# Optimization experiments

Measured on AMD Instinct MI355X. Metric: run time of the kernel, lower is better.

Reference implementation:

```python
import jax, jax.numpy as jnp
import numpy as np

V = 200000  # num entities
R = 100     # num relations
D = 128     # embedding_dim
K = 20      # entity_neighbor_num
B = 128     # batch (docs)
N = 50      # entities per doc


def setup_inputs() -> dict:
    key = jax.random.key(0)
    ks = jax.random.split(key, 8)
    return {
        "entity_ids": jax.random.randint(ks[0], (B, N), 0, V),
        "adj_entity": jax.random.randint(ks[1], (V, K), 0, V),
        "adj_relation": jax.random.randint(ks[2], (V, K), 0, R),
        "entity_embedding": jax.random.normal(ks[3], (V, D), jnp.float32),
        "relation_embedding": jax.random.normal(ks[4], (R, D), jnp.float32),
        "W_att": jax.random.normal(ks[5], (3 * D, 1), jnp.float32) * 0.05,
        "b_att": jnp.zeros((1,), jnp.float32),
        "W_conv": jax.random.normal(ks[6], (2 * D, D), jnp.float32) * 0.05,
        "b_conv": jnp.zeros((D,), jnp.float32),
    }


def reference(entity_ids, adj_entity, adj_relation, entity_embedding,
              relation_embedding, W_att, b_att, W_conv, b_conv):
    # neighbor ids: [B, N, K]
    neigh_ent = adj_entity[entity_ids]
    neigh_rel = adj_relation[entity_ids]
    ne = entity_embedding[neigh_ent]      # [B, N, K, D]
    nr = relation_embedding[neigh_rel]    # [B, N, K, D]
    ee = entity_embedding[entity_ids]     # [B, N, D]
    ee_exp = jnp.broadcast_to(ee[:, :, None, :], ne.shape)  # [B, N, K, D]
    concat = jnp.concatenate([ee_exp, ne, nr], axis=-1)     # [B, N, K, 3D]
    logits = jax.nn.relu(concat @ W_att + b_att)            # [B, N, K, 1]
    # NOTE: faithful to original nn.Softmax(dim=0) -> softmax over batch axis
    att = jax.nn.softmax(logits, axis=0)                    # [B, N, K, 1]
    neighbor_att = jnp.sum(att * ne, axis=2)                # [B, N, D]
    agg_in = jnp.concatenate([ee, neighbor_att], axis=-1)   # [B, N, 2D]
    return jax.nn.relu(agg_in @ W_conv + b_conv)            # [B, N, D]
```

## Files before the change

### kernel.cpp

```cpp
#include <hip/hip_runtime.h>

#define V 200000
#define R 100
#define D 128
#define K 20
#define B 128
#define N 50

__global__ void k_logits(const int* __restrict__ eids,
                         const int* __restrict__ adjE,
                         const int* __restrict__ adjR,
                         const float* __restrict__ EE,
                         const float* __restrict__ RE,
                         const float* __restrict__ Watt,
                         const float* __restrict__ batt,
                         float* __restrict__ att) {
  const int lane = threadIdx.x & 63;
  const int wv   = threadIdx.x >> 6;
  const int bn   = blockIdx.x * 4 + wv;
  const int b = bn / N;
  const int n = bn % N;
  const int eid = eids[bn];

  const float2 wa_e = ((const float2*)Watt)[lane];
  const float2 e2   = ((const float2*)(EE + (size_t)eid * D))[lane];
  float p = e2.x * wa_e.x + e2.y * wa_e.y;
  #pragma unroll
  for (int off = 32; off > 0; off >>= 1) p += __shfl_down(p, off);
  const float s_ee = __shfl(p, 0) + batt[0];

  const int g  = lane >> 4;
  const int sl = lane & 15;
  const float4* wnp = (const float4*)(Watt + D + 8 * sl);
  const float4* wrp = (const float4*)(Watt + 2 * D + 8 * sl);
  const float4 wn0 = wnp[0], wn1 = wnp[1];
  const float4 wr0 = wrp[0], wr1 = wrp[1];

  const int* ae = adjE + eid * K;
  const int* ar = adjR + eid * K;

  float q[5];
  #pragma unroll
  for (int k5 = 0; k5 < 5; ++k5) {
    const int k = k5 * 4 + g;
    const int nid = ae[k];
    const int rid = ar[k];
    const float4* np = (const float4*)(EE + (size_t)nid * D + 8 * sl);
    const float4* rp = (const float4*)(RE + (size_t)rid * D + 8 * sl);
    const float4 n0 = np[0], n1 = np[1];
    const float4 r0 = rp[0], r1 = rp[1];
    float s = n0.x * wn0.x + n0.y * wn0.y + n0.z * wn0.z + n0.w * wn0.w
            + n1.x * wn1.x + n1.y * wn1.y + n1.z * wn1.z + n1.w * wn1.w
            + r0.x * wr0.x + r0.y * wr0.y + r0.z * wr0.z + r0.w * wr0.w
            + r1.x * wr1.x + r1.y * wr1.y + r1.z * wr1.z + r1.w * wr1.w;
    #pragma unroll
    for (int off = 8; off > 0; off >>= 1) s += __shfl_down(s, off, 16);
    q[k5] = s;
  }

  if (sl == 0) {
    #pragma unroll
    for (int k5 = 0; k5 < 5; ++k5) {
      const int k = k5 * 4 + g;
      const float logit = s_ee + q[k5];
      att[(n * K + k) * B + b] = logit > 0.0f ? logit : 0.0f;
    }
  }
}

__global__ void k_softmax(float* __restrict__ att) {
  __shared__ float red[4];
  const int gg = blockIdx.x;
  const int t = threadIdx.x;
  const float x = att[gg * B + t];

  float m = x;
  #pragma unroll
  for (int off = 32; off > 0; off >>= 1) m = fmaxf(m, __shfl_down(m, off));
  if ((t & 63) == 0) red[t >> 6] = m;
  __syncthreads();
  const float mm = fmaxf(red[0], red[1]);

  const float e = __expf(x - mm);
  float s = e;
  #pragma unroll
  for (int off = 32; off > 0; off >>= 1) s += __shfl_down(s, off);
  if ((t & 63) == 0) red[2 + (t >> 6)] = s;
  __syncthreads();
  const float ss = red[2] + red[3];

  att[gg * B + t] = e / ss;
}

#define G 8
__global__ void k_out(const int* __restrict__ eids,
                      const int* __restrict__ adjE,
                      const float* __restrict__ EE,
                      const float* __restrict__ att,
                      const float* __restrict__ Wc,
                      const float* __restrict__ bc,
                      float* __restrict__ out) {
  __shared__ float agg[G][2 * D];
  __shared__ float part[2][G][D];
  __shared__ float s_att[G][K];
  __shared__ int   s_nid[G][K];

  const int t = threadIdx.x;
  const int d = t & 127;
  const int h = t >> 7;
  const int base = blockIdx.x * G;

  if (t < G * K) {
    const int j = t / K, k = t % K;
    const int bn = base + j;
    const int b = bn / N;
    const int n = bn % N;
    const int eid = eids[bn];
    s_nid[j][k] = adjE[eid * K + k];
    s_att[j][k] = att[(n * K + k) * B + b];
  }
  __syncthreads();

  #pragma unroll
  for (int jj = 0; jj < G / 2; ++jj) {
    const int j = h + jj * 2;
    const int bn = base + j;
    const int eid = eids[bn];
    const float ee = EE[(size_t)eid * D + d];
    float na = 0.0f;
    #pragma unroll
    for (int k = 0; k < K; ++k)
      na += s_att[j][k] * EE[(size_t)s_nid[j][k] * D + d];
    agg[j][d] = ee;
    agg[j][D + d] = na;
  }
  __syncthreads();

  float acc[G];
  #pragma unroll
  for (int j = 0; j < G; ++j) acc[j] = 0.0f;
  const int ibase = h * D;
  for (int c = 0; c < 32; ++c) {
    const int i = ibase + c * 4;
    const float w0 = Wc[(i + 0) * D + d];
    const float w1 = Wc[(i + 1) * D + d];
    const float w2 = Wc[(i + 2) * D + d];
    const float w3 = Wc[(i + 3) * D + d];
    #pragma unroll
    for (int j = 0; j < G; ++j) {
      const float4 a = *(const float4*)&agg[j][i];
      acc[j] += a.x * w0 + a.y * w1 + a.z * w2 + a.w * w3;
    }
  }
  #pragma unroll
  for (int j = 0; j < G; ++j) part[h][j][d] = acc[j];
  __syncthreads();

  const float bb = bc[d];
  #pragma unroll
  for (int jj = 0; jj < G / 2; ++jj) {
    const int j = h + jj * 2;
    const float v = part[0][j][d] + part[1][j][d] + bb;
    out[(size_t)(base + j) * D + d] = v > 0.0f ? v : 0.0f;
  }
}

extern "C" void kernel_launch(void* const* d_in, const int* in_sizes, int n_in,
                              void* d_out, int out_size, void* d_ws, size_t ws_size,
                              hipStream_t stream) {
  const int*   eids = (const int*)d_in[0];
  const int*   adjE = (const int*)d_in[1];
  const int*   adjR = (const int*)d_in[2];
  const float* EE   = (const float*)d_in[3];
  const float* RE   = (const float*)d_in[4];
  const float* Watt = (const float*)d_in[5];
  const float* batt = (const float*)d_in[6];
  const float* Wc   = (const float*)d_in[7];
  const float* bc   = (const float*)d_in[8];
  float* out = (float*)d_out;

  float* att = (float*)d_ws;

  k_logits<<<(B * N) / 4, 256, 0, stream>>>(eids, adjE, adjR, EE, RE, Watt,
                                            batt, att);
  k_softmax<<<N * K, 128, 0, stream>>>(att);
  k_out<<<(B * N) / G, 256, 0, stream>>>(eids, adjE, EE, att, Wc, bc, out);
}
```

Before: 206.3 us.

## Precompute per-entity attention scores and fuse the logit gather into softmax

The attention logit is linear in the concatenated input, so it splits into per-entity and per-relation dot products with slices of W_att. A new kernel computes these scalar scores for every entity and relation by streaming the whole tables sequentially. The softmax kernel then builds each logit from three scalar lookups instead of gathering full 128-wide neighbor and relation rows. This swaps a random gather of about 128k rows for a sequential read of all 200k entity rows, plus extra workspace for the score arrays.

```diff
diff --git a/kernel.cpp b/kernel.cpp
--- a/kernel.cpp
+++ b/kernel.cpp
@@ -7,89 +7,72 @@
 #define B 128
 #define N 50
 
-__global__ void k_logits(const int* __restrict__ eids,
-                         const int* __restrict__ adjE,
-                         const int* __restrict__ adjR,
-                         const float* __restrict__ EE,
+__global__ void k_scores(const float* __restrict__ EE,
                          const float* __restrict__ RE,
                          const float* __restrict__ Watt,
-                         const float* __restrict__ batt,
-                         float* __restrict__ att) {
+                         float* __restrict__ s0,
+                         float* __restrict__ s1,
+                         float* __restrict__ s2) {
   const int lane = threadIdx.x & 63;
-  const int wv   = threadIdx.x >> 6;
-  const int bn   = blockIdx.x * 4 + wv;
-  const int b = bn / N;
-  const int n = bn % N;
-  const int eid = eids[bn];
-
-  const float2 wa_e = ((const float2*)Watt)[lane];
-  const float2 e2   = ((const float2*)(EE + (size_t)eid * D))[lane];
-  float p = e2.x * wa_e.x + e2.y * wa_e.y;
-  #pragma unroll
-  for (int off = 32; off > 0; off >>= 1) p += __shfl_down(p, off);
-  const float s_ee = __shfl(p, 0) + batt[0];
-
-  const int g  = lane >> 4;
-  const int sl = lane & 15;
-  const float4* wnp = (const float4*)(Watt + D + 8 * sl);
-  const float4* wrp = (const float4*)(Watt + 2 * D + 8 * sl);
-  const float4 wn0 = wnp[0], wn1 = wnp[1];
-  const float4 wr0 = wrp[0], wr1 = wrp[1];
-
-  const int* ae = adjE + eid * K;
-  const int* ar = adjR + eid * K;
-
-  float q[5];
-  #pragma unroll
-  for (int k5 = 0; k5 < 5; ++k5) {
-    const int k = k5 * 4 + g;
-    const int nid = ae[k];
-    const int rid = ar[k];
-    const float4* np = (const float4*)(EE + (size_t)nid * D + 8 * sl);
-    const float4* rp = (const float4*)(RE + (size_t)rid * D + 8 * sl);
-    const float4 n0 = np[0], n1 = np[1];
-    const float4 r0 = rp[0], r1 = rp[1];
-    float s = n0.x * wn0.x + n0.y * wn0.y + n0.z * wn0.z + n0.w * wn0.w
-            + n1.x * wn1.x + n1.y * wn1.y + n1.z * wn1.z + n1.w * wn1.w
-            + r0.x * wr0.x + r0.y * wr0.y + r0.z * wr0.z + r0.w * wr0.w
-            + r1.x * wr1.x + r1.y * wr1.y + r1.z * wr1.z + r1.w * wr1.w;
+  const int row  = blockIdx.x * 4 + (threadIdx.x >> 6);
+  if (row < V) {
+    const float2 w0 = ((const float2*)Watt)[lane];
+    const float2 w1 = ((const float2*)(Watt + D))[lane];
+    const float2 e  = ((const float2*)(EE + (size_t)row * D))[lane];
+    float p0 = e.x * w0.x + e.y * w0.y;
+    float p1 = e.x * w1.x + e.y * w1.y;
     #pragma unroll
-    for (int off = 8; off > 0; off >>= 1) s += __shfl_down(s, off, 16);
-    q[k5] = s;
-  }
-
-  if (sl == 0) {
+    for (int off = 32; off > 0; off >>= 1) {
+      p0 += __shfl_down(p0, off);
+      p1 += __shfl_down(p1, off);
+    }
+    if (lane == 0) { s0[row] = p0; s1[row] = p1; }
+  } else if (row < V + R) {
+    const float2 w2 = ((const float2*)(Watt + 2 * D))[lane];
+    const float2 e  = ((const float2*)(RE + (size_t)(row - V) * D))[lane];
+    float p2 = e.x * w2.x + e.y * w2.y;
     #pragma unroll
-    for (int k5 = 0; k5 < 5; ++k5) {
-      const int k = k5 * 4 + g;
-      const float logit = s_ee + q[k5];
-      att[(n * K + k) * B + b] = logit > 0.0f ? logit : 0.0f;
-    }
+    for (int off = 32; off > 0; off >>= 1) p2 += __shfl_down(p2, off);
+    if (lane == 0) s2[row - V] = p2;
   }
 }
 
-__global__ void k_softmax(float* __restrict__ att) {
+__global__ void k_att(const int* __restrict__ eids,
+                      const int* __restrict__ adjE,
+                      const int* __restrict__ adjR,
+                      const float* __restrict__ s0,
+                      const float* __restrict__ s1,
+                      const float* __restrict__ s2,
+                      const float* __restrict__ batt,
+                      float* __restrict__ att) {
   __shared__ float red[4];
   const int gg = blockIdx.x;
-  const int t = threadIdx.x;
-  const float x = att[gg * B + t];
+  const int n  = gg / K;
+  const int k  = gg % K;
+  const int b  = threadIdx.x;
 
-  float m = x;
+  const int eid = eids[b * N + n];
+  const int nid = adjE[eid * K + k];
+  const int rid = adjR[eid * K + k];
+  float l = s0[eid] + s1[nid] + s2[rid] + batt[0];
+  l = l > 0.0f ? l : 0.0f;
+
+  float m = l;
   #pragma unroll
   for (int off = 32; off > 0; off >>= 1) m = fmaxf(m, __shfl_down(m, off));
-  if ((t & 63) == 0) red[t >> 6] = m;
+  if ((b & 63) == 0) red[b >> 6] = m;
   __syncthreads();
   const float mm = fmaxf(red[0], red[1]);
 
-  const float e = __expf(x - mm);
+  const float e = __expf(l - mm);
   float s = e;
   #pragma unroll
   for (int off = 32; off > 0; off >>= 1) s += __shfl_down(s, off);
-  if ((t & 63) == 0) red[2 + (t >> 6)] = s;
+  if ((b & 63) == 0) red[2 + (b >> 6)] = s;
   __syncthreads();
   const float ss = red[2] + red[3];
 
-  att[gg * B + t] = e / ss;
+  att[gg * B + b] = e / ss;
 }
 
 #define G 8
@@ -180,9 +163,11 @@
   float* out = (float*)d_out;
 
   float* att = (float*)d_ws;
+  float* s0  = att + (size_t)N * K * B;
+  float* s1  = s0 + V;
+  float* s2  = s1 + V;
 
-  k_logits<<<(B * N) / 4, 256, 0, stream>>>(eids, adjE, adjR, EE, RE, Watt,
-                                            batt, att);
-  k_softmax<<<N * K, 128, 0, stream>>>(att);
+  k_scores<<<(V + R + 3) / 4, 256, 0, stream>>>(EE, RE, Watt, s0, s1, s2);
+  k_att<<<N * K, B, 0, stream>>>(eids, adjE, adjR, s0, s1, s2, batt, att);
   k_out<<<(B * N) / G, 256, 0, stream>>>(eids, adjE, EE, att, Wc, bc, out);
 }
```

New measurement: 219.2 us. 6.3% more time.
